# Kernel tuning notes

Hardware: AMD Instinct MI355X
Metric: run time of the kernel (lower is better)

Reference implementation:

```python
import jax, jax.numpy as jnp
import numpy as np

B, H, D, HD = 16384, 8, 256, 128  # batch, heads, dim, hidden_dim


def setup_inputs() -> dict:
    key = jax.random.key(0)
    ks = jax.random.split(key, 8)
    return {
        "x": jax.random.normal(ks[0], (B, D), dtype=jnp.float32),
        "h": jax.random.normal(ks[1], (B, H, HD), dtype=jnp.float32),
        "sigmoid_w": jax.random.normal(ks[2], (H, HD + D, 2), dtype=jnp.float32),
        "sigmoid_b": jax.random.normal(ks[3], (H, 2), dtype=jnp.float32),
        "tanh_w": jax.random.normal(ks[4], (H, HD + D, HD), dtype=jnp.float32),
        "tanh_b": jax.random.normal(ks[5], (H, HD), dtype=jnp.float32),
        "out_w": jax.random.normal(ks[6], (H, HD, D), dtype=jnp.float32),
        "out_b": jax.random.normal(ks[7], (H, D), dtype=jnp.float32),
    }


def reference(x, h, sigmoid_w, sigmoid_b, tanh_w, tanh_b, out_w, out_b):
    # x: [B, D] -> broadcast across heads: [B, H, D]
    x_ = jnp.broadcast_to(x[:, None, :], (x.shape[0], h.shape[1], x.shape[1]))
    # gate input: [B, H, hidden+dim]
    sig_in = jnp.concatenate([h, x_], axis=2)
    sigmoids = jax.nn.sigmoid(jnp.einsum('bhm,hmn->bhn', sig_in, sigmoid_w) + sigmoid_b)
    # reset-gated hidden concat with x: [B, H, hidden+dim]
    tanh_in = jnp.concatenate([sigmoids[:, :, :1] * h, x_], axis=2)
    cand = jnp.tanh(jnp.einsum('bhm,hmn->bhn', tanh_in, tanh_w) + tanh_b)
    proportion = sigmoids[:, :, 1:]
    new_h = (1 - proportion) * h + proportion * cand
    output = jnp.einsum('bhm,hmn->bhn', new_h, out_w) + out_b
    return (output, new_h)
```

## Files before the change

### kernel.cpp

```cpp
#include <hip/hip_runtime.h>
#include <math.h>

typedef short bf16x8 __attribute__((ext_vector_type(8)));
typedef short bf16x4 __attribute__((ext_vector_type(4)));
typedef float floatx4 __attribute__((ext_vector_type(4)));
typedef float floatx2 __attribute__((ext_vector_type(2)));
typedef float floatx16 __attribute__((ext_vector_type(16)));

#define NB   16384
#define H8   8
#define ND   256
#define NHD  128
#define NK   384

__device__ __forceinline__ unsigned short f2bf(float f) {
  unsigned int u = __float_as_uint(f);
  u += 0x7FFFu + ((u >> 16) & 1u);
  return (unsigned short)(u >> 16);
}
__device__ __forceinline__ float bf2f(unsigned short s) {
  return __uint_as_float(((unsigned int)s) << 16);
}
__device__ __forceinline__ float fast_sigmoid(float z) {
  z = fminf(fmaxf(z, -60.f), 60.f);
  return __builtin_amdgcn_rcpf(1.f + __expf(-z));
}
__device__ __forceinline__ float fast_tanh(float s) {
  s = fminf(fmaxf(s, -9.f), 9.f);
  float e = __expf(2.f * s);
  return (e - 1.f) * __builtin_amdgcn_rcpf(e + 1.f);
}

#define WTP (H8 * 24 * 4 * 512)
#define WSP (H8 * 24 * 512)
#define WOP (H8 * 8 * 8 * 512)
#define XFP (NB * ND)
#define WS_NEED3 ((size_t)(2 * WTP + 2 * WSP + WOP + 2 * XFP) * 2)

__global__ void prep3b(const float* __restrict__ tanh_w,
                       const float* __restrict__ sig_w,
                       const float* __restrict__ out_w,
                       const float* __restrict__ x,
                       short* __restrict__ wtp_hi,
                       short* __restrict__ wsp_hi, short* __restrict__ wsp_lo,
                       short* __restrict__ wop,
                       short* __restrict__ xfh, short* __restrict__ xfl) {
  __shared__ float tile[16 * 260];
  const int t = threadIdx.x;
  const int b = blockIdx.x;
  if (b < 192) {
    int head = b / 24, ks = b % 24;
    const float* slab = tanh_w + ((size_t)head * NK + ks * 16) * NHD;
#pragma unroll
    for (int it = 0; it < 2; ++it) {
      int i = it * 256 + t;
      floatx4 v = reinterpret_cast<const floatx4*>(slab)[i];
      int r = i >> 5, c4 = i & 31;
      *reinterpret_cast<floatx4*>(&tile[r * 132 + c4 * 4]) = v;
    }
    __syncthreads();
    int ct = t >> 6, l = t & 63;
    bf16x8 hi8;
#pragma unroll
    for (int j = 0; j < 8; ++j) {
      float w = tile[((l >> 5) * 8 + j) * 132 + ct * 32 + (l & 31)];
      hi8[j] = (short)f2bf(w);
    }
    size_t dst = ((((size_t)head * 24 + ks) * 4 + ct) * 64 + l) * 8;
    *reinterpret_cast<bf16x8*>(wtp_hi + dst) = hi8;
  } else if (b < 256) {
    int head = (b - 192) / 8, ks = (b - 192) % 8;
    const float* slab = out_w + ((size_t)head * NHD + ks * 16) * ND;
#pragma unroll
    for (int it = 0; it < 4; ++it) {
      int i = it * 256 + t;
      floatx4 v = reinterpret_cast<const floatx4*>(slab)[i];
      int r = i >> 6, c4 = i & 63;
      *reinterpret_cast<floatx4*>(&tile[r * 260 + c4 * 4]) = v;
    }
    __syncthreads();
#pragma unroll
    for (int u = 0; u < 2; ++u) {
      int idx = u * 256 + t;
      int ct = idx >> 6, l = idx & 63;
      bf16x8 o8;
#pragma unroll
      for (int j = 0; j < 8; ++j) {
        float w = tile[((l >> 5) * 8 + j) * 260 + ct * 32 + (l & 31)];
        o8[j] = (short)f2bf(w);
      }
      size_t dst = ((((size_t)head * 8 + ks) * 8 + ct) * 64 + l) * 8;
      *reinterpret_cast<bf16x8*>(wop + dst) = o8;
    }
  } else {
    const int T2 = WSP;
    const int XQ8 = XFP / 8;
    for (int i = (b - 256) * 256 + t; i < T2 + XQ8; i += (gridDim.x - 256) * 256) {
      if (i < T2) {
        int j = i & 7, l = (i >> 3) & 63;
        int q = i >> 9;
        int ks = q % 24, head = q / 24;
        int k = ks * 16 + (l >> 5) * 8 + j, n = l & 31;
        float w = (n < 2) ? sig_w[((size_t)head * NK + k) * 2 + n] : 0.f;
        unsigned short hi = f2bf(w);
        wsp_hi[i] = (short)hi;
        wsp_lo[i] = (short)f2bf(w - bf2f(hi));
      } else {
        int q = i - T2;
        int bb = q >> 5, c0 = (q & 31) * 8;
        const float* xp = x + (size_t)bb * ND + c0;
        floatx4 v0 = *reinterpret_cast<const floatx4*>(xp);
        floatx4 v1 = *reinterpret_cast<const floatx4*>(xp + 4);
        bf16x8 h8, l8;
#pragma unroll
        for (int j = 0; j < 4; ++j) {
          unsigned short hb = f2bf(v0[j]);
          h8[j] = (short)hb; l8[j] = (short)f2bf(v0[j] - bf2f(hb));
          unsigned short hb2 = f2bf(v1[j]);
          h8[4 + j] = (short)hb2; l8[4 + j] = (short)f2bf(v1[j] - bf2f(hb2));
        }
        int dst = ((bb >> 5) * 16 + (c0 >> 4)) * 512 +
                  (((c0 >> 3) & 1) * 32 + (bb & 31)) * 8;
        *reinterpret_cast<bf16x8*>(xfh + dst) = h8;
        *reinterpret_cast<bf16x8*>(xfl + dst) = l8;
      }
    }
  }
}

__global__ __launch_bounds__(256, 4) void gru3(
    const float* __restrict__ h, const float* __restrict__ sig_b,
    const float* __restrict__ tanh_b, const float* __restrict__ out_b,
    const short* __restrict__ wtp_hi,
    const short* __restrict__ wsp_hi, const short* __restrict__ wsp_lo,
    const short* __restrict__ wop,
    const short* __restrict__ xfh, const short* __restrict__ xfl,
    float* __restrict__ out, float* __restrict__ out_nh) {
  __shared__ __align__(16) short AhH[16 * 512];
  __shared__ __align__(16) short AhL[16 * 512];
  __shared__ float sig_part[4 * 2 * 64];
  __shared__ float gbuf[64], pbuf[64];

  const int t = threadIdx.x;
  const int lane = t & 63;
  const int cq = t >> 6;
  const int l31 = lane & 31;
  const int lh = lane >> 5;
  const int head = (int)(blockIdx.x >> 8);
  const int rb = (int)(blockIdx.x & 255);
  const long rowbase = (long)rb * 64;

#pragma unroll
  for (int it = 0; it < 4; ++it) {
    int gi = it * 256 + t;
    int row = gi >> 4, kc = gi & 15;
    const float* hp = h + ((rowbase + row) * H8 + head) * NHD + kc * 8;
    floatx4 v0 = *reinterpret_cast<const floatx4*>(hp);
    floatx4 v1 = *reinterpret_cast<const floatx4*>(hp + 4);
    bf16x8 hi8, lo8;
#pragma unroll
    for (int j = 0; j < 4; ++j) {
      unsigned short hb = f2bf(v0[j]);
      hi8[j] = (short)hb; lo8[j] = (short)f2bf(v0[j] - bf2f(hb));
      unsigned short hb2 = f2bf(v1[j]);
      hi8[4 + j] = (short)hb2; lo8[4 + j] = (short)f2bf(v1[j] - bf2f(hb2));
    }
    int rg = row >> 5, row32 = row & 31;
    int chunk = (rg * 8 + (kc >> 1)) * 64 + (kc & 1) * 32 + row32;
    *reinterpret_cast<bf16x8*>(&AhH[chunk * 8]) = hi8;
    *reinterpret_cast<bf16x8*>(&AhL[chunk * 8]) = lo8;
  }
  __syncthreads();

  const short* __restrict__ sh_p = wsp_hi + ((size_t)head * 24 * 512) + lane * 8;
  const short* __restrict__ sl_p = wsp_lo + ((size_t)head * 24 * 512) + lane * 8;
  const short* __restrict__ xh0 = xfh + ((size_t)(rb * 2 + 0) * 16 * 512) + lane * 8;
  const short* __restrict__ xl0 = xfl + ((size_t)(rb * 2 + 0) * 16 * 512) + lane * 8;
  const short* __restrict__ xh1 = xfh + ((size_t)(rb * 2 + 1) * 16 * 512) + lane * 8;
  const short* __restrict__ xl1 = xfl + ((size_t)(rb * 2 + 1) * 16 * 512) + lane * 8;

  {
    floatx16 accS0, accS1;
#pragma unroll
    for (int z = 0; z < 16; ++z) { accS0[z] = 0.f; accS1[z] = 0.f; }
#pragma unroll
    for (int i = 0; i < 6; ++i) {
      int ks = cq * 6 + i;
      bf16x8 sh = *reinterpret_cast<const bf16x8*>(sh_p + ks * 512);
      bf16x8 sl2 = *reinterpret_cast<const bf16x8*>(sl_p + ks * 512);
      bf16x8 a0h, a0l, a1h, a1l;
      if (ks < 8) {
        a0h = *reinterpret_cast<const bf16x8*>(&AhH[(ks * 64 + lane) * 8]);
        a0l = *reinterpret_cast<const bf16x8*>(&AhL[(ks * 64 + lane) * 8]);
        a1h = *reinterpret_cast<const bf16x8*>(&AhH[((8 + ks) * 64 + lane) * 8]);
        a1l = *reinterpret_cast<const bf16x8*>(&AhL[((8 + ks) * 64 + lane) * 8]);
      } else {
        int xk = ks - 8;
        a0h = *reinterpret_cast<const bf16x8*>(xh0 + xk * 512);
        a0l = *reinterpret_cast<const bf16x8*>(xl0 + xk * 512);
        a1h = *reinterpret_cast<const bf16x8*>(xh1 + xk * 512);
        a1l = *reinterpret_cast<const bf16x8*>(xl1 + xk * 512);
      }
      accS0 = __builtin_amdgcn_mfma_f32_32x32x16_bf16(a0h, sh, accS0, 0, 0, 0);
      accS0 = __builtin_amdgcn_mfma_f32_32x32x16_bf16(a0l, sh, accS0, 0, 0, 0);
      accS0 = __builtin_amdgcn_mfma_f32_32x32x16_bf16(a0h, sl2, accS0, 0, 0, 0);
      accS1 = __builtin_amdgcn_mfma_f32_32x32x16_bf16(a1h, sh, accS1, 0, 0, 0);
      accS1 = __builtin_amdgcn_mfma_f32_32x32x16_bf16(a1l, sh, accS1, 0, 0, 0);
      accS1 = __builtin_amdgcn_mfma_f32_32x32x16_bf16(a1h, sl2, accS1, 0, 0, 0);
    }
    if (l31 < 2) {
#pragma unroll
      for (int reg = 0; reg < 16; ++reg) {
        int crow = (reg & 3) + 8 * (reg >> 2) + 4 * lh;
        sig_part[(cq * 2 + l31) * 64 + crow] = accS0[reg];
        sig_part[(cq * 2 + l31) * 64 + 32 + crow] = accS1[reg];
      }
    }
  }
  __syncthreads();
  if (t < 128) {
    int r = t >> 1, colc = t & 1;
    float z = sig_part[(0 * 2 + colc) * 64 + r] +
              sig_part[(1 * 2 + colc) * 64 + r] +
              sig_part[(2 * 2 + colc) * 64 + r] +
              sig_part[(3 * 2 + colc) * 64 + r] +
              sig_b[head * 2 + colc];
    float s = fast_sigmoid(z);
    if (colc == 0) gbuf[r] = s; else pbuf[r] = s;
  }
  __syncthreads();

#pragma unroll
  for (int it = 0; it < 4; ++it) {
    int cidx = it * 256 + t;
    int fidx = cidx >> 6, lanec = cidx & 63;
    int row = (fidx >> 3) * 32 + (lanec & 31);
    float g = gbuf[row];
    bf16x8 hi8 = *reinterpret_cast<const bf16x8*>(&AhH[cidx * 8]);
    bf16x8 lo8 = *reinterpret_cast<const bf16x8*>(&AhL[cidx * 8]);
    bf16x8 nh8, nl8;
#pragma unroll
    for (int j = 0; j < 8; ++j) {
      float hv = bf2f((unsigned short)hi8[j]) + bf2f((unsigned short)lo8[j]);
      float s = g * hv;
      unsigned short hb = f2bf(s);
      nh8[j] = (short)hb;
      nl8[j] = (short)f2bf(s - bf2f(hb));
    }
    *reinterpret_cast<bf16x8*>(&AhH[cidx * 8]) = nh8;
    *reinterpret_cast<bf16x8*>(&AhL[cidx * 8]) = nl8;
  }
  __syncthreads();

  floatx16 acc0, acc1;
#pragma unroll
  for (int z = 0; z < 16; ++z) { acc0[z] = 0.f; acc1[z] = 0.f; }
  const short* __restrict__ bh_p = wtp_hi + (((size_t)head * 24 * 4 + cq) * 512) + lane * 8;

  bf16x8 bhA = *reinterpret_cast<const bf16x8*>(bh_p);
  bf16x8 bhB = *reinterpret_cast<const bf16x8*>(bh_p + 2048);
#pragma unroll
  for (int ks = 0; ks < 8; ++ks) {
    bf16x8 bh = bhA; bhA = bhB;
    bhB = *reinterpret_cast<const bf16x8*>(bh_p + (ks + 2) * 2048);
    bf16x8 a0h = *reinterpret_cast<const bf16x8*>(&AhH[(ks * 64 + lane) * 8]);
    bf16x8 a0l = *reinterpret_cast<const bf16x8*>(&AhL[(ks * 64 + lane) * 8]);
    bf16x8 a1h = *reinterpret_cast<const bf16x8*>(&AhH[((8 + ks) * 64 + lane) * 8]);
    bf16x8 a1l = *reinterpret_cast<const bf16x8*>(&AhL[((8 + ks) * 64 + lane) * 8]);
    acc0 = __builtin_amdgcn_mfma_f32_32x32x16_bf16(a0h, bh, acc0, 0, 0, 0);
    acc0 = __builtin_amdgcn_mfma_f32_32x32x16_bf16(a0l, bh, acc0, 0, 0, 0);
    acc1 = __builtin_amdgcn_mfma_f32_32x32x16_bf16(a1h, bh, acc1, 0, 0, 0);
    acc1 = __builtin_amdgcn_mfma_f32_32x32x16_bf16(a1l, bh, acc1, 0, 0, 0);
  }
  {
    bf16x8 x0A = *reinterpret_cast<const bf16x8*>(xh0);
    bf16x8 x1A = *reinterpret_cast<const bf16x8*>(xh1);
    bf16x8 x0B = *reinterpret_cast<const bf16x8*>(xh0 + 512);
    bf16x8 x1B = *reinterpret_cast<const bf16x8*>(xh1 + 512);
#pragma unroll
    for (int xk = 0; xk < 16; ++xk) {
      const int ks = 8 + xk;
      bf16x8 bh = bhA; bhA = bhB;
      if (ks + 2 < 24) bhB = *reinterpret_cast<const bf16x8*>(bh_p + (ks + 2) * 2048);
      bf16x8 x0 = x0A, x1 = x1A;
      x0A = x0B; x1A = x1B;
      if (xk + 2 < 16) {
        x0B = *reinterpret_cast<const bf16x8*>(xh0 + (xk + 2) * 512);
        x1B = *reinterpret_cast<const bf16x8*>(xh1 + (xk + 2) * 512);
      }
      acc0 = __builtin_amdgcn_mfma_f32_32x32x16_bf16(x0, bh, acc0, 0, 0, 0);
      acc1 = __builtin_amdgcn_mfma_f32_32x32x16_bf16(x1, bh, acc1, 0, 0, 0);
    }
  }
  __syncthreads();

  const int col = cq * 32 + l31;
  const float tb = tanh_b[head * NHD + col];
  const float* __restrict__ hcol = h + (rowbase * H8 + head) * NHD + col;
#define EPI(RG, ACC)                                                          \
  {                                                                           \
    _Pragma("unroll")                                                         \
    for (int reg = 0; reg < 16; ++reg) {                                      \
      int crow = (reg & 3) + 8 * (reg >> 2) + 4 * lh;                         \
      int row = RG * 32 + crow;                                               \
      float p = pbuf[row];                                                    \
      float cand = fast_tanh(ACC[reg] + tb);                                  \
      float hv = hcol[(size_t)row * (H8 * NHD)];                              \
      float nh = hv + p * (cand - hv);                                        \
      int el = ((RG * 8 + (col >> 4)) * 64 + ((l31 >> 3) & 1) * 32 + crow) * 8 + (col & 7); \
      out_nh[((rowbase + row) * H8 + head) * NHD + col] = nh;                 \
      AhH[el] = (short)f2bf(nh);                                              \
    }                                                                         \
  }
  EPI(0, acc0)
  EPI(1, acc1)
#undef EPI
  __syncthreads();

  const short* __restrict__ wo_p = wop + (((size_t)head * 64 + cq * 2) * 512) + lane * 8;
  const float ob0 = out_b[head * ND + cq * 64 + l31];
  const float ob1 = out_b[head * ND + cq * 64 + 32 + l31];
#define OUTP(RG)                                                              \
  {                                                                           \
    floatx16 a3a, a3b;                                                        \
    _Pragma("unroll")                                                         \
    for (int z = 0; z < 16; ++z) { a3a[z] = 0.f; a3b[z] = 0.f; }              \
    bf16x8 w0n = *reinterpret_cast<const bf16x8*>(wo_p);                      \
    bf16x8 w1n = *reinterpret_cast<const bf16x8*>(wo_p + 512);                \
    _Pragma("unroll")                                                         \
    for (int ks = 0; ks < 8; ++ks) {                                          \
      bf16x8 w0 = w0n, w1 = w1n;                                              \
      if (ks < 7) {                                                           \
        w0n = *reinterpret_cast<const bf16x8*>(wo_p + (ks + 1) * 4096);       \
        w1n = *reinterpret_cast<const bf16x8*>(wo_p + (ks + 1) * 4096 + 512); \
      }                                                                       \
      bf16x8 a = *reinterpret_cast<const bf16x8*>(&AhH[((RG * 8 + ks) * 64 + lane) * 8]); \
      a3a = __builtin_amdgcn_mfma_f32_32x32x16_bf16(a, w0, a3a, 0, 0, 0);     \
      a3b = __builtin_amdgcn_mfma_f32_32x32x16_bf16(a, w1, a3b, 0, 0, 0);     \
    }                                                                         \
    _Pragma("unroll")                                                         \
    for (int reg = 0; reg < 16; ++reg) {                                      \
      int row = RG * 32 + (reg & 3) + 8 * (reg >> 2) + 4 * lh;                \
      long obase = ((rowbase + row) * H8 + head) * ND;                        \
      out[obase + cq * 64 + l31] = a3a[reg] + ob0;                            \
      out[obase + cq * 64 + 32 + l31] = a3b[reg] + ob1;                       \
    }                                                                         \
  }
  OUTP(0)
  OUTP(1)
#undef OUTP
}

#define WT_ELEMS (H8 * NK * NHD)
#define WO_ELEMS (H8 * NHD * ND)

__global__ void prep_kernel(const float* __restrict__ tanh_w,
                            const float* __restrict__ out_w,
                            short* __restrict__ wt_hi,
                            short* __restrict__ wt_lo,
                            short* __restrict__ wo) {
  const int total1 = WT_ELEMS;
  const int total2 = WO_ELEMS;
  for (int i = blockIdx.x * blockDim.x + threadIdx.x; i < total1 + total2;
       i += gridDim.x * blockDim.x) {
    if (i < total1) {
      int hh = i / (NK * NHD);
      int rem = i - hh * NK * NHD;
      int k = rem / NHD, n = rem - k * NHD;
      float w = tanh_w[i];
      unsigned short hi = f2bf(w);
      unsigned short lo = f2bf(w - bf2f(hi));
      int dst = hh * (48 * NHD * 8) + (k >> 3) * (NHD * 8) + n * 8 + (k & 7);
      wt_hi[dst] = (short)hi;
      wt_lo[dst] = (short)lo;
    } else {
      int j = i - total1;
      int hh = j / (NHD * ND);
      int rem = j - hh * NHD * ND;
      int k = rem / ND, n = rem - k * ND;
      int dst = hh * (16 * ND * 8) + (k >> 3) * (ND * 8) + n * 8 + (k & 7);
      wo[dst] = (short)f2bf(out_w[j]);
    }
  }
}

#define BM   32
#define NT   512
#define LDA 392
#define LDNH 136

__global__ __launch_bounds__(NT, 4) void gru_main(
    const float* __restrict__ x, const float* __restrict__ h,
    const float* __restrict__ sig_w, const float* __restrict__ sig_b,
    const float* __restrict__ tanh_b, const float* __restrict__ out_b,
    const short* __restrict__ wt_hi, const short* __restrict__ wt_lo,
    const short* __restrict__ wo,
    float* __restrict__ out, float* __restrict__ out_nh) {
  __shared__ __align__(16) short Ahi[BM][LDA];
  __shared__ __align__(16) short Alo[BM][LDA];
  __shared__ __align__(16) short NHL[BM][LDNH];
  __shared__ floatx2 swl[NK];
  __shared__ float gbuf[BM], pbuf[BM];

  const int t = threadIdx.x;
  const int lane = t & 63;
  const int wid = t >> 6;
  const int wrow = wid >> 2;
  const int wcol = wid & 3;
  const int ln = lane & 15;
  const int kg = lane >> 4;
  const int head = blockIdx.x & 7;
  const long rowbase = (long)(blockIdx.x >> 3) * BM;
  const int arow = wrow * 16 + ln;

#pragma unroll
  for (int i = 0; i < 4; ++i) {
    int idx = i * NT + t;
    int r = idx >> 6, c4 = idx & 63;
    floatx4 v = *reinterpret_cast<const floatx4*>(x + (rowbase + r) * ND + c4 * 4);
    bf16x4 hi, lo;
#pragma unroll
    for (int j = 0; j < 4; ++j) {
      unsigned short hb = f2bf(v[j]);
      hi[j] = (short)hb;
      lo[j] = (short)f2bf(v[j] - bf2f(hb));
    }
    *reinterpret_cast<bf16x4*>(&Ahi[r][NHD + c4 * 4]) = hi;
    *reinterpret_cast<bf16x4*>(&Alo[r][NHD + c4 * 4]) = lo;
  }
#pragma unroll
  for (int i = 0; i < 2; ++i) {
    int idx = i * NT + t;
    int r = idx >> 5, c4 = idx & 31;
    floatx4 v = *reinterpret_cast<const floatx4*>(
        h + ((rowbase + r) * H8 + head) * NHD + c4 * 4);
    bf16x4 hi, lo;
#pragma unroll
    for (int j = 0; j < 4; ++j) {
      unsigned short hb = f2bf(v[j]);
      hi[j] = (short)hb;
      lo[j] = (short)f2bf(v[j] - bf2f(hb));
    }
    *reinterpret_cast<bf16x4*>(&Ahi[r][c4 * 4]) = hi;
    *reinterpret_cast<bf16x4*>(&Alo[r][c4 * 4]) = lo;
  }
  if (t < NK)
    swl[t] = *reinterpret_cast<const floatx2*>(sig_w + ((size_t)head * NK + t) * 2);
  __syncthreads();
  {
    int r = t >> 4, u = t & 15;
    float a0 = 0.f, a1 = 0.f;
#pragma unroll
    for (int kk = 0; kk < 24; ++kk) {
      int k = u + kk * 16;
      float a = bf2f((unsigned short)Ahi[r][k]) + bf2f((unsigned short)Alo[r][k]);
      floatx2 w = swl[k];
      a0 += a * w[0];
      a1 += a * w[1];
    }
#pragma unroll
    for (int off = 1; off < 16; off <<= 1) {
      a0 += __shfl_xor(a0, off);
      a1 += __shfl_xor(a1, off);
    }
    if (u == 0) {
      gbuf[r] = fast_sigmoid(a0 + sig_b[head * 2 + 0]);
      pbuf[r] = fast_sigmoid(a1 + sig_b[head * 2 + 1]);
    }
  }
  floatx4 acc1[2] = {{0.f, 0.f, 0.f, 0.f}, {0.f, 0.f, 0.f, 0.f}};
  floatx4 acc2[2] = {{0.f, 0.f, 0.f, 0.f}, {0.f, 0.f, 0.f, 0.f}};
  const size_t wtbase = (size_t)head * (48 * NHD * 8);
#pragma unroll
  for (int ks = 0; ks < 12; ++ks) {
    bf16x8 ahi = *reinterpret_cast<const bf16x8*>(&Ahi[arow][ks * 32 + kg * 8]);
    bf16x8 alo = *reinterpret_cast<const bf16x8*>(&Alo[arow][ks * 32 + kg * 8]);
    floatx4* acc = (ks < 4) ? acc1 : acc2;
#pragma unroll
    for (int cf = 0; cf < 2; ++cf) {
      int n0 = wcol * 32 + cf * 16;
      size_t woff = wtbase + (size_t)(ks * 4 + kg) * (NHD * 8) + (size_t)(n0 + ln) * 8;
      bf16x8 bhi = *reinterpret_cast<const bf16x8*>(wt_hi + woff);
      bf16x8 blo = *reinterpret_cast<const bf16x8*>(wt_lo + woff);
      acc[cf] = __builtin_amdgcn_mfma_f32_16x16x32_bf16(ahi, bhi, acc[cf], 0, 0, 0);
      acc[cf] = __builtin_amdgcn_mfma_f32_16x16x32_bf16(alo, bhi, acc[cf], 0, 0, 0);
      acc[cf] = __builtin_amdgcn_mfma_f32_16x16x32_bf16(ahi, blo, acc[cf], 0, 0, 0);
    }
  }
  __syncthreads();
#pragma unroll
  for (int cf = 0; cf < 2; ++cf) {
    int col = wcol * 32 + cf * 16 + ln;
    float tb = tanh_b[head * NHD + col];
#pragma unroll
    for (int j = 0; j < 4; ++j) {
      int r = wrow * 16 + kg * 4 + j;
      float g = gbuf[r], p = pbuf[r];
      float s = g * acc1[cf][j] + acc2[cf][j] + tb;
      float cand = fast_tanh(s);
      float hv = bf2f((unsigned short)Ahi[r][col]) + bf2f((unsigned short)Alo[r][col]);
      float nh = hv + p * (cand - hv);
      out_nh[((rowbase + r) * H8 + head) * NHD + col] = nh;
      NHL[r][col] = (short)f2bf(nh);
    }
  }
  __syncthreads();
  floatx4 acc3[4] = {{0.f, 0.f, 0.f, 0.f}, {0.f, 0.f, 0.f, 0.f},
                     {0.f, 0.f, 0.f, 0.f}, {0.f, 0.f, 0.f, 0.f}};
  const size_t wobase = (size_t)head * (16 * ND * 8);
#pragma unroll
  for (int ks = 0; ks < 4; ++ks) {
    bf16x8 a = *reinterpret_cast<const bf16x8*>(&NHL[arow][ks * 32 + kg * 8]);
#pragma unroll
    for (int cf = 0; cf < 4; ++cf) {
      int n0 = wcol * 64 + cf * 16;
      size_t woff = wobase + (size_t)(ks * 4 + kg) * (ND * 8) + (size_t)(n0 + ln) * 8;
      bf16x8 bfr = *reinterpret_cast<const bf16x8*>(wo + woff);
      acc3[cf] = __builtin_amdgcn_mfma_f32_16x16x32_bf16(a, bfr, acc3[cf], 0, 0, 0);
    }
  }
#pragma unroll
  for (int cf = 0; cf < 4; ++cf) {
    int col = wcol * 64 + cf * 16 + ln;
    float ob = out_b[head * ND + col];
#pragma unroll
    for (int j = 0; j < 4; ++j) {
      int r = wrow * 16 + kg * 4 + j;
      out[((rowbase + r) * H8 + head) * ND + col] = acc3[cf][j] + ob;
    }
  }
}

extern "C" void kernel_launch(void* const* d_in, const int* in_sizes, int n_in,
                              void* d_out, int out_size, void* d_ws, size_t ws_size,
                              hipStream_t stream) {
  (void)in_sizes; (void)n_in; (void)out_size;
  const float* x      = (const float*)d_in[0];
  const float* h      = (const float*)d_in[1];
  const float* sig_w  = (const float*)d_in[2];
  const float* sig_b  = (const float*)d_in[3];
  const float* tanh_w = (const float*)d_in[4];
  const float* tanh_b = (const float*)d_in[5];
  const float* out_w  = (const float*)d_in[6];
  const float* out_b  = (const float*)d_in[7];

  float* out = (float*)d_out;
  float* out_nh = out + (size_t)NB * H8 * ND;

  if (ws_size >= WS_NEED3) {
    short* wtp_hi = (short*)d_ws;
    short* wtp_lo = wtp_hi + WTP;
    short* wsp_hi = wtp_lo + WTP;
    short* wsp_lo = wsp_hi + WSP;
    short* wop    = wsp_lo + WSP;
    short* xfh    = wop + WOP;
    short* xfl    = xfh + XFP;
    hipLaunchKernelGGL(prep3b, dim3(256 + 2432), dim3(256), 0, stream,
                       tanh_w, sig_w, out_w, x,
                       wtp_hi, wsp_hi, wsp_lo, wop, xfh, xfl);
    hipLaunchKernelGGL(gru3, dim3((NB / 64) * H8), dim3(256), 0, stream,
                       h, sig_b, tanh_b, out_b,
                       wtp_hi, wsp_hi, wsp_lo, wop, xfh, xfl,
                       out, out_nh);
  } else {
    short* wt_hi = (short*)d_ws;
    short* wt_lo = wt_hi + WT_ELEMS;
    short* wo    = wt_lo + WT_ELEMS;
    hipLaunchKernelGGL(prep_kernel, dim3(512), dim3(256), 0, stream,
                       tanh_w, out_w, wt_hi, wt_lo, wo);
    hipLaunchKernelGGL(gru_main, dim3((NB / BM) * H8), dim3(NT), 0, stream,
                       x, h, sig_w, sig_b, tanh_b, out_b, wt_hi, wt_lo, wo,
                       out, out_nh);
  }
}
```

Baseline: 95.44 us.

## Compute sigmoid gates in fp32 during prep and drop split-bf16 gate MFMA

Sigmoid gate projections move out of the main GRU kernel. They are now computed in fp32 with scalar FMAs by extra blocks of the prep kernel and written to workspace gate arrays, which the main kernel reads to scale h as it loads it. This removes the hi/lo bf16 gate MFMA loop, two barriers and the in-LDS rescale pass from the main kernel. It also drops the x low-part conversion and storage, cutting workspace traffic. The cost is an extra full read of h in the prep kernel, plus gate-array writes and reads.

```diff
diff --git a/kernel.cpp b/kernel.cpp
--- a/kernel.cpp
+++ b/kernel.cpp
@@ -32,23 +32,26 @@
 }
 
 #define WTP (H8 * 24 * 4 * 512)
-#define WSP (H8 * 24 * 512)
 #define WOP (H8 * 8 * 8 * 512)
 #define XFP (NB * ND)
-#define WS_NEED3 ((size_t)(2 * WTP + 2 * WSP + WOP + 2 * XFP) * 2)
-
-__global__ void prep3b(const float* __restrict__ tanh_w,
+#define NGATE (NB * H8)
+#define WS_NEED3 ((size_t)(WTP + WOP + XFP) * 2 + (size_t)2 * NGATE * 4)
+
+__global__ void prep3c(const float* __restrict__ tanh_w,
                        const float* __restrict__ sig_w,
+                       const float* __restrict__ sig_b,
                        const float* __restrict__ out_w,
                        const float* __restrict__ x,
+                       const float* __restrict__ h,
                        short* __restrict__ wtp_hi,
-                       short* __restrict__ wsp_hi, short* __restrict__ wsp_lo,
                        short* __restrict__ wop,
-                       short* __restrict__ xfh, short* __restrict__ xfl) {
-  __shared__ float tile[16 * 260];
+                       short* __restrict__ xfh,
+                       float* __restrict__ gW, float* __restrict__ pW) {
+  __shared__ float smem[14480];
   const int t = threadIdx.x;
   const int b = blockIdx.x;
   if (b < 192) {
+    float* tile = smem;
     int head = b / 24, ks = b % 24;
     const float* slab = tanh_w + ((size_t)head * NK + ks * 16) * NHD;
 #pragma unroll
@@ -69,6 +72,7 @@
     size_t dst = ((((size_t)head * 24 + ks) * 4 + ct) * 64 + l) * 8;
     *reinterpret_cast<bf16x8*>(wtp_hi + dst) = hi8;
   } else if (b < 256) {
+    float* tile = smem;
     int head = (b - 192) / 8, ks = (b - 192) % 8;
     const float* slab = out_w + ((size_t)head * NHD + ks * 16) * ND;
 #pragma unroll
@@ -92,54 +96,83 @@
       size_t dst = ((((size_t)head * 8 + ks) * 8 + ct) * 64 + l) * 8;
       *reinterpret_cast<bf16x8*>(wop + dst) = o8;
     }
+  } else if (b < 2304) {
+    int i = (b - 256) * 256 + t;
+    int bb = i >> 5, c0 = (i & 31) * 8;
+    const float* xp = x + (size_t)bb * ND + c0;
+    floatx4 v0 = *reinterpret_cast<const floatx4*>(xp);
+    floatx4 v1 = *reinterpret_cast<const floatx4*>(xp + 4);
+    bf16x8 h8;
+#pragma unroll
+    for (int j = 0; j < 4; ++j) {
+      h8[j] = (short)f2bf(v0[j]);
+      h8[4 + j] = (short)f2bf(v1[j]);
+    }
+    int dst = ((bb >> 5) * 16 + (c0 >> 4)) * 512 +
+              (((c0 >> 3) & 1) * 32 + (bb & 31)) * 8;
+    *reinterpret_cast<bf16x8*>(xfh + dst) = h8;
   } else {
-    const int T2 = WSP;
-    const int XQ8 = XFP / 8;
-    for (int i = (b - 256) * 256 + t; i < T2 + XQ8; i += (gridDim.x - 256) * 256) {
-      if (i < T2) {
-        int j = i & 7, l = (i >> 3) & 63;
-        int q = i >> 9;
-        int ks = q % 24, head = q / 24;
-        int k = ks * 16 + (l >> 5) * 8 + j, n = l & 31;
-        float w = (n < 2) ? sig_w[((size_t)head * NK + k) * 2 + n] : 0.f;
-        unsigned short hi = f2bf(w);
-        wsp_hi[i] = (short)hi;
-        wsp_lo[i] = (short)f2bf(w - bf2f(hi));
-      } else {
-        int q = i - T2;
-        int bb = q >> 5, c0 = (q & 31) * 8;
-        const float* xp = x + (size_t)bb * ND + c0;
-        floatx4 v0 = *reinterpret_cast<const floatx4*>(xp);
-        floatx4 v1 = *reinterpret_cast<const floatx4*>(xp + 4);
-        bf16x8 h8, l8;
-#pragma unroll
-        for (int j = 0; j < 4; ++j) {
-          unsigned short hb = f2bf(v0[j]);
-          h8[j] = (short)hb; l8[j] = (short)f2bf(v0[j] - bf2f(hb));
-          unsigned short hb2 = f2bf(v1[j]);
-          h8[4 + j] = (short)hb2; l8[4 + j] = (short)f2bf(v1[j] - bf2f(hb2));
-        }
-        int dst = ((bb >> 5) * 16 + (c0 >> 4)) * 512 +
-                  (((c0 >> 3) & 1) * 32 + (bb & 31)) * 8;
-        *reinterpret_cast<bf16x8*>(xfh + dst) = h8;
-        *reinterpret_cast<bf16x8*>(xfl + dst) = l8;
+    float* xs = smem;
+    float* ws = smem + 8320;
+    int gb = b - 2304;
+    long rowb = (long)gb * 32;
+#pragma unroll
+    for (int it = 0; it < 8; ++it) {
+      int idx = it * 256 + t;
+      int r = idx >> 6, c4 = idx & 63;
+      floatx4 v = *reinterpret_cast<const floatx4*>(x + (rowb + r) * ND + c4 * 4);
+      *reinterpret_cast<floatx4*>(&xs[r * 260 + c4 * 4]) = v;
+    }
+#pragma unroll
+    for (int it = 0; it < 12; ++it) {
+      int idx = it * 256 + t;
+      floatx2 v = *reinterpret_cast<const floatx2*>(sig_w + (size_t)idx * 2);
+      int head = idx / 384;
+      int rem = idx * 2 - head * 768;
+      *reinterpret_cast<floatx2*>(&ws[head * 770 + rem]) = v;
+    }
+    __syncthreads();
+    int bl = t >> 3, head = t & 7;
+    const float* hrow = h + (rowb * 8 + t) * 128;
+    const float* wh = &ws[head * 770];
+    float a0 = 0.f, a1 = 0.f;
+#pragma unroll 8
+    for (int k4 = 0; k4 < 32; ++k4) {
+      floatx4 hv = *reinterpret_cast<const floatx4*>(hrow + k4 * 4);
+#pragma unroll
+      for (int j = 0; j < 4; ++j) {
+        floatx2 w2 = *reinterpret_cast<const floatx2*>(&wh[(k4 * 4 + j) * 2]);
+        a0 += hv[j] * w2[0];
+        a1 += hv[j] * w2[1];
       }
     }
+    const float* xrow = &xs[bl * 260];
+#pragma unroll 8
+    for (int k4 = 0; k4 < 64; ++k4) {
+      floatx4 xv = *reinterpret_cast<const floatx4*>(xrow + k4 * 4);
+#pragma unroll
+      for (int j = 0; j < 4; ++j) {
+        floatx2 w2 = *reinterpret_cast<const floatx2*>(&wh[(128 + k4 * 4 + j) * 2]);
+        a0 += xv[j] * w2[0];
+        a1 += xv[j] * w2[1];
+      }
+    }
+    long gi = rowb * 8 + t;
+    gW[gi] = fast_sigmoid(a0 + sig_b[head * 2 + 0]);
+    pW[gi] = fast_sigmoid(a1 + sig_b[head * 2 + 1]);
   }
 }
 
 __global__ __launch_bounds__(256, 4) void gru3(
-    const float* __restrict__ h, const float* __restrict__ sig_b,
+    const float* __restrict__ h,
     const float* __restrict__ tanh_b, const float* __restrict__ out_b,
-    const short* __restrict__ wtp_hi,
-    const short* __restrict__ wsp_hi, const short* __restrict__ wsp_lo,
-    const short* __restrict__ wop,
-    const short* __restrict__ xfh, const short* __restrict__ xfl,
+    const short* __restrict__ wtp_hi, const short* __restrict__ wop,
+    const short* __restrict__ xfh,
+    const float* __restrict__ gW, const float* __restrict__ pW,
     float* __restrict__ out, float* __restrict__ out_nh) {
   __shared__ __align__(16) short AhH[16 * 512];
   __shared__ __align__(16) short AhL[16 * 512];
-  __shared__ float sig_part[4 * 2 * 64];
-  __shared__ float gbuf[64], pbuf[64];
+  __shared__ float pbuf[64];
 
   const int t = threadIdx.x;
   const int lane = t & 63;
@@ -150,20 +183,25 @@
   const int rb = (int)(blockIdx.x & 255);
   const long rowbase = (long)rb * 64;
 
+  if (t < 64) pbuf[t] = pW[(rowbase + t) * H8 + head];
+
 #pragma unroll
   for (int it = 0; it < 4; ++it) {
     int gi = it * 256 + t;
     int row = gi >> 4, kc = gi & 15;
+    float g = gW[(rowbase + row) * H8 + head];
     const float* hp = h + ((rowbase + row) * H8 + head) * NHD + kc * 8;
     floatx4 v0 = *reinterpret_cast<const floatx4*>(hp);
     floatx4 v1 = *reinterpret_cast<const floatx4*>(hp + 4);
     bf16x8 hi8, lo8;
 #pragma unroll
     for (int j = 0; j < 4; ++j) {
-      unsigned short hb = f2bf(v0[j]);
-      hi8[j] = (short)hb; lo8[j] = (short)f2bf(v0[j] - bf2f(hb));
-      unsigned short hb2 = f2bf(v1[j]);
-      hi8[4 + j] = (short)hb2; lo8[4 + j] = (short)f2bf(v1[j] - bf2f(hb2));
+      float s0 = g * v0[j];
+      unsigned short hb = f2bf(s0);
+      hi8[j] = (short)hb; lo8[j] = (short)f2bf(s0 - bf2f(hb));
+      float s1 = g * v1[j];
+      unsigned short hb2 = f2bf(s1);
+      hi8[4 + j] = (short)hb2; lo8[4 + j] = (short)f2bf(s1 - bf2f(hb2));
     }
     int rg = row >> 5, row32 = row & 31;
     int chunk = (rg * 8 + (kc >> 1)) * 64 + (kc & 1) * 32 + row32;
@@ -172,90 +210,13 @@
   }
   __syncthreads();
 
-  const short* __restrict__ sh_p = wsp_hi + ((size_t)head * 24 * 512) + lane * 8;
-  const short* __restrict__ sl_p = wsp_lo + ((size_t)head * 24 * 512) + lane * 8;
   const short* __restrict__ xh0 = xfh + ((size_t)(rb * 2 + 0) * 16 * 512) + lane * 8;
-  const short* __restrict__ xl0 = xfl + ((size_t)(rb * 2 + 0) * 16 * 512) + lane * 8;
   const short* __restrict__ xh1 = xfh + ((size_t)(rb * 2 + 1) * 16 * 512) + lane * 8;
-  const short* __restrict__ xl1 = xfl + ((size_t)(rb * 2 + 1) * 16 * 512) + lane * 8;
-
-  {
-    floatx16 accS0, accS1;
-#pragma unroll
-    for (int z = 0; z < 16; ++z) { accS0[z] = 0.f; accS1[z] = 0.f; }
-#pragma unroll
-    for (int i = 0; i < 6; ++i) {
-      int ks = cq * 6 + i;
-      bf16x8 sh = *reinterpret_cast<const bf16x8*>(sh_p + ks * 512);
-      bf16x8 sl2 = *reinterpret_cast<const bf16x8*>(sl_p + ks * 512);
-      bf16x8 a0h, a0l, a1h, a1l;
-      if (ks < 8) {
-        a0h = *reinterpret_cast<const bf16x8*>(&AhH[(ks * 64 + lane) * 8]);
-        a0l = *reinterpret_cast<const bf16x8*>(&AhL[(ks * 64 + lane) * 8]);
-        a1h = *reinterpret_cast<const bf16x8*>(&AhH[((8 + ks) * 64 + lane) * 8]);
-        a1l = *reinterpret_cast<const bf16x8*>(&AhL[((8 + ks) * 64 + lane) * 8]);
-      } else {
-        int xk = ks - 8;
-        a0h = *reinterpret_cast<const bf16x8*>(xh0 + xk * 512);
-        a0l = *reinterpret_cast<const bf16x8*>(xl0 + xk * 512);
-        a1h = *reinterpret_cast<const bf16x8*>(xh1 + xk * 512);
-        a1l = *reinterpret_cast<const bf16x8*>(xl1 + xk * 512);
-      }
-      accS0 = __builtin_amdgcn_mfma_f32_32x32x16_bf16(a0h, sh, accS0, 0, 0, 0);
-      accS0 = __builtin_amdgcn_mfma_f32_32x32x16_bf16(a0l, sh, accS0, 0, 0, 0);
-      accS0 = __builtin_amdgcn_mfma_f32_32x32x16_bf16(a0h, sl2, accS0, 0, 0, 0);
-      accS1 = __builtin_amdgcn_mfma_f32_32x32x16_bf16(a1h, sh, accS1, 0, 0, 0);
-      accS1 = __builtin_amdgcn_mfma_f32_32x32x16_bf16(a1l, sh, accS1, 0, 0, 0);
-      accS1 = __builtin_amdgcn_mfma_f32_32x32x16_bf16(a1h, sl2, accS1, 0, 0, 0);
-    }
-    if (l31 < 2) {
-#pragma unroll
-      for (int reg = 0; reg < 16; ++reg) {
-        int crow = (reg & 3) + 8 * (reg >> 2) + 4 * lh;
-        sig_part[(cq * 2 + l31) * 64 + crow] = accS0[reg];
-        sig_part[(cq * 2 + l31) * 64 + 32 + crow] = accS1[reg];
-      }
-    }
-  }
-  __syncthreads();
-  if (t < 128) {
-    int r = t >> 1, colc = t & 1;
-    float z = sig_part[(0 * 2 + colc) * 64 + r] +
-              sig_part[(1 * 2 + colc) * 64 + r] +
-              sig_part[(2 * 2 + colc) * 64 + r] +
-              sig_part[(3 * 2 + colc) * 64 + r] +
-              sig_b[head * 2 + colc];
-    float s = fast_sigmoid(z);
-    if (colc == 0) gbuf[r] = s; else pbuf[r] = s;
-  }
-  __syncthreads();
-
-#pragma unroll
-  for (int it = 0; it < 4; ++it) {
-    int cidx = it * 256 + t;
-    int fidx = cidx >> 6, lanec = cidx & 63;
-    int row = (fidx >> 3) * 32 + (lanec & 31);
-    float g = gbuf[row];
-    bf16x8 hi8 = *reinterpret_cast<const bf16x8*>(&AhH[cidx * 8]);
-    bf16x8 lo8 = *reinterpret_cast<const bf16x8*>(&AhL[cidx * 8]);
-    bf16x8 nh8, nl8;
-#pragma unroll
-    for (int j = 0; j < 8; ++j) {
-      float hv = bf2f((unsigned short)hi8[j]) + bf2f((unsigned short)lo8[j]);
-      float s = g * hv;
-      unsigned short hb = f2bf(s);
-      nh8[j] = (short)hb;
-      nl8[j] = (short)f2bf(s - bf2f(hb));
-    }
-    *reinterpret_cast<bf16x8*>(&AhH[cidx * 8]) = nh8;
-    *reinterpret_cast<bf16x8*>(&AhL[cidx * 8]) = nl8;
-  }
-  __syncthreads();
+  const short* __restrict__ bh_p = wtp_hi + (((size_t)head * 24 * 4 + cq) * 512) + lane * 8;
 
   floatx16 acc0, acc1;
 #pragma unroll
   for (int z = 0; z < 16; ++z) { acc0[z] = 0.f; acc1[z] = 0.f; }
-  const short* __restrict__ bh_p = wtp_hi + (((size_t)head * 24 * 4 + cq) * 512) + lane * 8;
 
   bf16x8 bhA = *reinterpret_cast<const bf16x8*>(bh_p);
   bf16x8 bhB = *reinterpret_cast<const bf16x8*>(bh_p + 2048);
@@ -549,18 +510,15 @@
 
   if (ws_size >= WS_NEED3) {
     short* wtp_hi = (short*)d_ws;
-    short* wtp_lo = wtp_hi + WTP;
-    short* wsp_hi = wtp_lo + WTP;
-    short* wsp_lo = wsp_hi + WSP;
-    short* wop    = wsp_lo + WSP;
+    short* wop    = wtp_hi + WTP;
     short* xfh    = wop + WOP;
-    short* xfl    = xfh + XFP;
-    hipLaunchKernelGGL(prep3b, dim3(256 + 2432), dim3(256), 0, stream,
-                       tanh_w, sig_w, out_w, x,
-                       wtp_hi, wsp_hi, wsp_lo, wop, xfh, xfl);
+    float* gW     = (float*)(xfh + XFP);
+    float* pW     = gW + NGATE;
+    hipLaunchKernelGGL(prep3c, dim3(256 + 2048 + 512), dim3(256), 0, stream,
+                       tanh_w, sig_w, sig_b, out_w, x, h,
+                       wtp_hi, wop, xfh, gW, pW);
     hipLaunchKernelGGL(gru3, dim3((NB / 64) * H8), dim3(256), 0, stream,
-                       h, sig_b, tanh_b, out_b,
-                       wtp_hi, wsp_hi, wsp_lo, wop, xfh, xfl,
+                       h, tanh_b, out_b, wtp_hi, wop, xfh, gW, pW,
                        out, out_nh);
   } else {
     short* wt_hi = (short*)d_ws;
```

After: 92.12 us. -3.5%, faster.
